# Optimization experiments

Measured on AMD Instinct MI355X. Metric: run time of the kernel, lower is better.

The kernel has to match this reference:

```python
import jax, jax.numpy as jnp
import numpy as np

H = 512   # hidden_size
B = 32    # batch
S = 2048  # src_len
NEG = -1e10


def setup_inputs() -> dict:
    key = jax.random.key(0)
    k1, k2, k3, k4, k5, k6 = jax.random.split(key, 6)
    hidden = jax.random.normal(k1, (B, 2 * H), dtype=jnp.float32)
    encoder_outputs = jax.random.normal(k2, (S, B, 2 * H), dtype=jnp.float32)
    mask = jax.random.randint(k3, (B, S), 0, 2, dtype=jnp.int32)
    # params: nn.Linear(4H, H) -> weight [H, 4H], bias [H]; v ~ U[0,1) [H]
    bound = 1.0 / np.sqrt(4 * H)
    attn_w = jax.random.uniform(k4, (H, 4 * H), minval=-bound, maxval=bound, dtype=jnp.float32)
    attn_b = jax.random.uniform(k5, (H,), minval=-bound, maxval=bound, dtype=jnp.float32)
    v = jax.random.uniform(k6, (H,), dtype=jnp.float32)
    return {"hidden": hidden, "encoder_outputs": encoder_outputs, "mask": mask,
            "attn_w": attn_w, "attn_b": attn_b, "v": v}


def reference(hidden, encoder_outputs, mask, attn_w, attn_b, v):
    # hidden: [B, 2H] -> [B, S, 2H]; encoder_outputs: [S, B, 2H] -> [B, S, 2H]
    src_len = encoder_outputs.shape[0]
    h = jnp.broadcast_to(hidden[:, None, :], (hidden.shape[0], src_len, hidden.shape[1]))
    eo = jnp.transpose(encoder_outputs, (1, 0, 2))
    cat = jnp.concatenate((h, eo), axis=2)                      # [B, S, 4H]
    energy = jnp.tanh(jnp.einsum('bsf,hf->bsh', cat, attn_w) + attn_b)  # [B, S, H]
    attention = jnp.einsum('bsh,h->bs', energy, v)              # [B, S]
    attention = jnp.where(mask == 0, NEG, attention)
    return jax.nn.softmax(attention, axis=1)
```

## Files before the change

### kernel.cpp

```cpp
#include <hip/hip_runtime.h>

#define SLEN 2048
#define BATCH 32
#define HDIM 512
#define KDIM 1024

typedef _Float16 f16x8 __attribute__((ext_vector_type(8)));
typedef _Float16 f16x4 __attribute__((ext_vector_type(4)));
typedef float f32x4 __attribute__((ext_vector_type(4)));

__device__ __forceinline__ void gload16(const void* g, void* l) {
  __builtin_amdgcn_global_load_lds(
      (const __attribute__((address_space(1))) unsigned int*)g,
      (__attribute__((address_space(3))) unsigned int*)l, 16, 0, 0);
}

__device__ __forceinline__ float fast_tanh(float x) {
  float e = __expf(2.0f * x);
  return 1.0f - 2.0f * __builtin_amdgcn_rcpf(e + 1.0f);
}

__global__ __launch_bounds__(256) void prep_k(const float* __restrict__ attn_w,
                                              const float* __restrict__ attn_b,
                                              const float* __restrict__ hidden,
                                              _Float16* __restrict__ Bt,
                                              float* __restrict__ s1,
                                              float* __restrict__ score) {
  if (blockIdx.x < 512) {
    int t = blockIdx.x * 256 + threadIdx.x;
    int h = t >> 8;
    int c = t & 255;
    float4 x = *(const float4*)(attn_w + (size_t)h * 2048 + 1024 + c * 4);
    f16x4 y = {(_Float16)x.x, (_Float16)x.y, (_Float16)x.z, (_Float16)x.w};
    *(f16x4*)(Bt + (size_t)h * 1024 + c * 4) = y;
  } else if (blockIdx.x < 4608) {
    int o = (blockIdx.x - 512) * 4 + (threadIdx.x >> 6);
    int b = o >> 9, h = o & 511;
    int lane = threadIdx.x & 63;
    const float4* hp = (const float4*)(hidden + (size_t)b * 1024);
    const float4* wp = (const float4*)(attn_w + (size_t)h * 2048);
    float acc = 0.f;
#pragma unroll
    for (int c = 0; c < 4; ++c) {
      float4 a = hp[c * 64 + lane];
      float4 wv = wp[c * 64 + lane];
      acc += a.x * wv.x + a.y * wv.y + a.z * wv.z + a.w * wv.w;
    }
#pragma unroll
    for (int off = 1; off < 64; off <<= 1) acc += __shfl_xor(acc, off);
    if (lane == 0) s1[o] = acc + attn_b[h];
  } else {
    int idx = (blockIdx.x - 4608) * 256 + threadIdx.x;
    float4 z = {0.f, 0.f, 0.f, 0.f};
    ((float4*)score)[idx] = z;
    ((float4*)score)[idx + 8192] = z;
  }
}

__global__ __launch_bounds__(256, 2) void gemm_k(const float* __restrict__ eo,
                                                 const _Float16* __restrict__ Bt,
                                                 const float* __restrict__ s1,
                                                 const float* __restrict__ v,
                                                 float* __restrict__ score) {
  constexpr int BK = 32;
  constexpr int NKT = KDIM / BK;
  __shared__ __align__(16) float As[2][256 * BK];
  __shared__ __align__(16) _Float16 Bs[2][128 * BK];

  int bid = blockIdx.x;
  int x = bid & 7;
  int q = bid >> 3;
  int nt = q & 3;
  int mt = (q >> 2) * 8 + x;

  int tid = threadIdx.x;
  int lane = tid & 63;
  int w = tid >> 6;
  int wm = w * 64;

  const float* ga[8];
  const _Float16* gb[2];
#pragma unroll
  for (int i = 0; i < 8; ++i)
    ga[i] = eo + (size_t)(mt * 256 + 64 * w + 8 * i + (lane >> 3)) * KDIM
              + (((lane & 7) ^ (lane >> 3)) << 2);
  gb[0] = Bt + (size_t)(nt * 128 + 32 * w + (lane >> 2)) * KDIM
            + (((lane & 3) ^ (lane >> 4)) << 3);
  gb[1] = gb[0] + 16 * KDIM;

  f32x4 acc[4][8];
#pragma unroll
  for (int i = 0; i < 4; ++i)
#pragma unroll
    for (int j = 0; j < 8; ++j) acc[i][j] = (f32x4){0.f, 0.f, 0.f, 0.f};

  int mrow = lane & 15;
  int quad = lane >> 4;
  int bchunk = (quad ^ (mrow >> 2)) & 3;
  int as_sw = mrow & 7;

  {
    gload16(gb[0], (char*)Bs[0] + (w * 2 + 0) * 1024);
    gload16(gb[1], (char*)Bs[0] + (w * 2 + 1) * 1024);
    gb[0] += BK; gb[1] += BK;
#pragma unroll
    for (int i = 0; i < 8; ++i) {
      gload16(ga[i], (char*)As[0] + (w * 8 + i) * 1024);
      ga[i] += BK;
    }
  }

  for (int kt = 0; kt < NKT; ++kt) {
    int cur = kt & 1;

    if (kt + 1 < NKT) {
      gload16(gb[0], (char*)Bs[cur ^ 1] + (w * 2 + 0) * 1024);
      gload16(gb[1], (char*)Bs[cur ^ 1] + (w * 2 + 1) * 1024);
      gb[0] += BK; gb[1] += BK;
#pragma unroll
      for (int i = 0; i < 8; ++i) {
        gload16(ga[i], (char*)As[cur ^ 1] + (w * 8 + i) * 1024);
        ga[i] += BK;
      }
      asm volatile("s_waitcnt vmcnt(10)" ::: "memory");
    } else {
      asm volatile("s_waitcnt vmcnt(0)" ::: "memory");
    }
    __builtin_amdgcn_s_barrier();

    const float* Ab = As[cur];
    const _Float16* Bb = Bs[cur];
    f16x8 bf[8], af[4];
#pragma unroll
    for (int j = 0; j < 8; ++j)
      bf[j] = *(const f16x8*)&Bb[(16 * j + mrow) * BK + (bchunk << 3)];
#pragma unroll
    for (int i = 0; i < 4; ++i) {
      const float* pa = &Ab[(wm + 16 * i + mrow) * BK];
      float4 a0 = *(const float4*)(pa + (((2 * quad) ^ as_sw) << 2));
      float4 a1 = *(const float4*)(pa + (((2 * quad + 1) ^ as_sw) << 2));
      f16x8 t = {(_Float16)a0.x, (_Float16)a0.y, (_Float16)a0.z, (_Float16)a0.w,
                 (_Float16)a1.x, (_Float16)a1.y, (_Float16)a1.z, (_Float16)a1.w};
      af[i] = t;
    }
    asm volatile("s_waitcnt lgkmcnt(0)" ::: "memory");
    __builtin_amdgcn_sched_barrier(0);
    __builtin_amdgcn_s_barrier();

    __builtin_amdgcn_s_setprio(1);
#pragma unroll
    for (int i = 0; i < 4; ++i)
#pragma unroll
      for (int j = 0; j < 8; ++j)
        acc[i][j] = __builtin_amdgcn_mfma_f32_16x16x32_f16(af[i], bf[j], acc[i][j], 0, 0, 0);
    __builtin_amdgcn_s_setprio(0);
  }

  __syncthreads();
  float* s1s = (float*)As;
  float* vsm = (float*)Bs;
  for (int t = tid; t < 1024; t += 256) {
    int bb = t >> 5, cc = t & 31;
    ((float4*)s1s)[bb * 33 + cc] = *(const float4*)(s1 + (size_t)bb * 512 + nt * 128 + cc * 4);
  }
  if (tid < 32) ((float4*)vsm)[tid] = *(const float4*)(v + nt * 128 + tid * 4);
  __syncthreads();

  int lcol = lane & 15;
  float vv[8];
#pragma unroll
  for (int j = 0; j < 8; ++j) vv[j] = vsm[16 * j + lcol];

#pragma unroll
  for (int i = 0; i < 4; ++i) {
#pragma unroll
    for (int r = 0; r < 4; ++r) {
      int mloc = wm + 16 * i + 4 * quad + r;
      int bb = mloc & 31;
      float sum = 0.f;
#pragma unroll
      for (int j = 0; j < 8; ++j) {
        float e = acc[i][j][r] + s1s[bb * 132 + 16 * j + lcol];
        sum += fast_tanh(e) * vv[j];
      }
      sum += __shfl_xor(sum, 1);
      sum += __shfl_xor(sum, 2);
      sum += __shfl_xor(sum, 4);
      sum += __shfl_xor(sum, 8);
      if (lcol == 0) {
        int mg = mt * 256 + mloc;
        atomicAdd(&score[(mg & 31) * SLEN + (mg >> 5)], sum);
      }
    }
  }
}

__global__ __launch_bounds__(256) void softmax_k(const float* __restrict__ score,
                                                 const int* __restrict__ mask,
                                                 float* __restrict__ out) {
  int b = blockIdx.x;
  int tid = threadIdx.x;
  int lane = tid & 63, w = tid >> 6;
  __shared__ float red[8];
  float vals[8];
  float mx = -3.4e38f;
#pragma unroll
  for (int i = 0; i < 8; ++i) {
    int s = i * 256 + tid;
    float xv = score[b * SLEN + s];
    if (mask[b * SLEN + s] == 0) xv = -1e10f;
    vals[i] = xv;
    mx = fmaxf(mx, xv);
  }
#pragma unroll
  for (int off = 1; off < 64; off <<= 1) mx = fmaxf(mx, __shfl_xor(mx, off));
  if (lane == 0) red[w] = mx;
  __syncthreads();
  mx = fmaxf(fmaxf(red[0], red[1]), fmaxf(red[2], red[3]));
  float sum = 0.f;
#pragma unroll
  for (int i = 0; i < 8; ++i) {
    vals[i] = __expf(vals[i] - mx);
    sum += vals[i];
  }
#pragma unroll
  for (int off = 1; off < 64; off <<= 1) sum += __shfl_xor(sum, off);
  if (lane == 0) red[4 + w] = sum;
  __syncthreads();
  sum = red[4] + red[5] + red[6] + red[7];
  float inv = 1.0f / sum;
#pragma unroll
  for (int i = 0; i < 8; ++i) out[b * SLEN + i * 256 + tid] = vals[i] * inv;
}

extern "C" void kernel_launch(void* const* d_in, const int* in_sizes, int n_in,
                              void* d_out, int out_size, void* d_ws, size_t ws_size,
                              hipStream_t stream) {
  const float* hidden = (const float*)d_in[0];
  const float* eo     = (const float*)d_in[1];
  const int*   mask   = (const int*)d_in[2];
  const float* attn_w = (const float*)d_in[3];
  const float* attn_b = (const float*)d_in[4];
  const float* v      = (const float*)d_in[5];
  float* out = (float*)d_out;

  char* wsb = (char*)d_ws;
  _Float16* Bt = (_Float16*)wsb;
  float* s1    = (float*)(wsb + (1 << 20));
  float* score = (float*)(wsb + (1 << 20) + (1 << 16));

  prep_k<<<4640, 256, 0, stream>>>(attn_w, attn_b, hidden, Bt, s1, score);
  gemm_k<<<1024, 256, 0, stream>>>(eo, Bt, s1, v, score);
  softmax_k<<<BATCH, 256, 0, stream>>>(score, mask, out);
}
```

Measured before the change: 449.4 us.

## Pre-convert encoder outputs to fp16 and retile GEMM with triple buffering

Adds a prep stage that converts the full encoder_outputs tensor to fp16 in workspace. The GEMM then loads fp16 A tiles directly instead of fp32 tiles that had to be converted in registers. The GEMM tile shrinks from 256x128 to 128x128 with a 2x2 warp layout, LDS becomes a 3-stage ring buffer, and occupancy is raised to 3 blocks per CU. This trades an extra full read of eo plus a 128MB fp16 write and re-read for half the LDS and global traffic inside the GEMM and deeper prefetch; the grid doubles, which also doubles the number of atomic adds into the score buffer.

```diff
diff --git a/kernel.cpp b/kernel.cpp
--- a/kernel.cpp
+++ b/kernel.cpp
@@ -23,9 +23,11 @@
 __global__ __launch_bounds__(256) void prep_k(const float* __restrict__ attn_w,
                                               const float* __restrict__ attn_b,
                                               const float* __restrict__ hidden,
+                                              const float* __restrict__ eo,
                                               _Float16* __restrict__ Bt,
                                               float* __restrict__ s1,
-                                              float* __restrict__ score) {
+                                              float* __restrict__ score,
+                                              _Float16* __restrict__ eo16) {
   if (blockIdx.x < 512) {
     int t = blockIdx.x * 256 + threadIdx.x;
     int h = t >> 8;
@@ -49,23 +51,34 @@
 #pragma unroll
     for (int off = 1; off < 64; off <<= 1) acc += __shfl_xor(acc, off);
     if (lane == 0) s1[o] = acc + attn_b[h];
-  } else {
+  } else if (blockIdx.x < 4640) {
     int idx = (blockIdx.x - 4608) * 256 + threadIdx.x;
     float4 z = {0.f, 0.f, 0.f, 0.f};
     ((float4*)score)[idx] = z;
     ((float4*)score)[idx + 8192] = z;
-  }
-}
-
-__global__ __launch_bounds__(256, 2) void gemm_k(const float* __restrict__ eo,
+  } else {
+    int g = (blockIdx.x - 4640) * 256 + threadIdx.x;
+    const float4* src = (const float4*)eo;
+#pragma unroll
+    for (int it = 0; it < 16; ++it) {
+      size_t c = (size_t)it * 524288 + g;
+      float4 a = src[c * 2];
+      float4 b2 = src[c * 2 + 1];
+      f16x8 o = {(_Float16)a.x,  (_Float16)a.y,  (_Float16)a.z,  (_Float16)a.w,
+                 (_Float16)b2.x, (_Float16)b2.y, (_Float16)b2.z, (_Float16)b2.w};
+      *(f16x8*)(eo16 + c * 8) = o;
+    }
+  }
+}
+
+__global__ __launch_bounds__(256, 3) void gemm_k(const _Float16* __restrict__ eo16,
                                                  const _Float16* __restrict__ Bt,
                                                  const float* __restrict__ s1,
                                                  const float* __restrict__ v,
                                                  float* __restrict__ score) {
   constexpr int BK = 32;
   constexpr int NKT = KDIM / BK;
-  __shared__ __align__(16) float As[2][256 * BK];
-  __shared__ __align__(16) _Float16 Bs[2][128 * BK];
+  __shared__ __align__(16) char smem[49152];
 
   int bid = blockIdx.x;
   int x = bid & 7;
@@ -76,73 +89,63 @@
   int tid = threadIdx.x;
   int lane = tid & 63;
   int w = tid >> 6;
-  int wm = w * 64;
-
-  const float* ga[8];
+  int wm = (w >> 1) * 64;
+  int wn = (w & 1) * 64;
+
+  const _Float16* ga[2];
   const _Float16* gb[2];
-#pragma unroll
-  for (int i = 0; i < 8; ++i)
-    ga[i] = eo + (size_t)(mt * 256 + 64 * w + 8 * i + (lane >> 3)) * KDIM
-              + (((lane & 7) ^ (lane >> 3)) << 2);
-  gb[0] = Bt + (size_t)(nt * 128 + 32 * w + (lane >> 2)) * KDIM
-            + (((lane & 3) ^ (lane >> 4)) << 3);
-  gb[1] = gb[0] + 16 * KDIM;
-
-  f32x4 acc[4][8];
+  int swz = ((lane & 3) ^ ((lane >> 3) & 3)) << 3;
+#pragma unroll
+  for (int i = 0; i < 2; ++i) {
+    ga[i] = eo16 + (size_t)(mt * 128 + 32 * w + 16 * i + (lane >> 2)) * KDIM + swz;
+    gb[i] = Bt + (size_t)(nt * 128 + 32 * w + 16 * i + (lane >> 2)) * KDIM + swz;
+  }
+
+  f32x4 acc[4][4];
 #pragma unroll
   for (int i = 0; i < 4; ++i)
 #pragma unroll
-    for (int j = 0; j < 8; ++j) acc[i][j] = (f32x4){0.f, 0.f, 0.f, 0.f};
+    for (int j = 0; j < 4; ++j) acc[i][j] = (f32x4){0.f, 0.f, 0.f, 0.f};
 
   int mrow = lane & 15;
   int quad = lane >> 4;
-  int bchunk = (quad ^ (mrow >> 2)) & 3;
-  int as_sw = mrow & 7;
-
-  {
-    gload16(gb[0], (char*)Bs[0] + (w * 2 + 0) * 1024);
-    gload16(gb[1], (char*)Bs[0] + (w * 2 + 1) * 1024);
-    gb[0] += BK; gb[1] += BK;
-#pragma unroll
-    for (int i = 0; i < 8; ++i) {
-      gload16(ga[i], (char*)As[0] + (w * 8 + i) * 1024);
-      ga[i] += BK;
-    }
-  }
-
+  int rc = (quad ^ ((mrow >> 1) & 3)) << 3;
+
+#define STAGE(buf)                                                    \
+  {                                                                   \
+    gload16(ga[0], smem + (buf)*8192 + (w * 2 + 0) * 1024);           \
+    gload16(ga[1], smem + (buf)*8192 + (w * 2 + 1) * 1024);           \
+    ga[0] += BK; ga[1] += BK;                                         \
+    gload16(gb[0], smem + 24576 + (buf)*8192 + (w * 2 + 0) * 1024);   \
+    gload16(gb[1], smem + 24576 + (buf)*8192 + (w * 2 + 1) * 1024);   \
+    gb[0] += BK; gb[1] += BK;                                         \
+  }
+
+  STAGE(0);
+  STAGE(1);
+
+  int cur = 0, nx2 = 2;
   for (int kt = 0; kt < NKT; ++kt) {
-    int cur = kt & 1;
-
-    if (kt + 1 < NKT) {
-      gload16(gb[0], (char*)Bs[cur ^ 1] + (w * 2 + 0) * 1024);
-      gload16(gb[1], (char*)Bs[cur ^ 1] + (w * 2 + 1) * 1024);
-      gb[0] += BK; gb[1] += BK;
-#pragma unroll
-      for (int i = 0; i < 8; ++i) {
-        gload16(ga[i], (char*)As[cur ^ 1] + (w * 8 + i) * 1024);
-        ga[i] += BK;
-      }
-      asm volatile("s_waitcnt vmcnt(10)" ::: "memory");
+    if (kt + 2 < NKT) {
+      STAGE(nx2);
+      asm volatile("s_waitcnt vmcnt(8)" ::: "memory");
+    } else if (kt + 1 < NKT) {
+      asm volatile("s_waitcnt vmcnt(4)" ::: "memory");
     } else {
       asm volatile("s_waitcnt vmcnt(0)" ::: "memory");
     }
     __builtin_amdgcn_s_barrier();
 
-    const float* Ab = As[cur];
-    const _Float16* Bb = Bs[cur];
-    f16x8 bf[8], af[4];
-#pragma unroll
-    for (int j = 0; j < 8; ++j)
-      bf[j] = *(const f16x8*)&Bb[(16 * j + mrow) * BK + (bchunk << 3)];
-#pragma unroll
-    for (int i = 0; i < 4; ++i) {
-      const float* pa = &Ab[(wm + 16 * i + mrow) * BK];
-      float4 a0 = *(const float4*)(pa + (((2 * quad) ^ as_sw) << 2));
-      float4 a1 = *(const float4*)(pa + (((2 * quad + 1) ^ as_sw) << 2));
-      f16x8 t = {(_Float16)a0.x, (_Float16)a0.y, (_Float16)a0.z, (_Float16)a0.w,
-                 (_Float16)a1.x, (_Float16)a1.y, (_Float16)a1.z, (_Float16)a1.w};
-      af[i] = t;
-    }
+    const _Float16* Ab = (const _Float16*)(smem + cur * 8192);
+    const _Float16* Bb = (const _Float16*)(smem + 24576 + cur * 8192);
+    f16x8 af[4], bf[4];
+#pragma unroll
+    for (int i = 0; i < 4; ++i)
+      af[i] = *(const f16x8*)&Ab[(wm + 16 * i + mrow) * BK + rc];
+#pragma unroll
+    for (int j = 0; j < 4; ++j)
+      bf[j] = *(const f16x8*)&Bb[(wn + 16 * j + mrow) * BK + rc];
+
     asm volatile("s_waitcnt lgkmcnt(0)" ::: "memory");
     __builtin_amdgcn_sched_barrier(0);
     __builtin_amdgcn_s_barrier();
@@ -151,14 +154,18 @@
 #pragma unroll
     for (int i = 0; i < 4; ++i)
 #pragma unroll
-      for (int j = 0; j < 8; ++j)
+      for (int j = 0; j < 4; ++j)
         acc[i][j] = __builtin_amdgcn_mfma_f32_16x16x32_f16(af[i], bf[j], acc[i][j], 0, 0, 0);
     __builtin_amdgcn_s_setprio(0);
-  }
-
-  __syncthreads();
-  float* s1s = (float*)As;
-  float* vsm = (float*)Bs;
+
+    cur = (cur == 2) ? 0 : cur + 1;
+    nx2 = (nx2 == 2) ? 0 : nx2 + 1;
+  }
+#undef STAGE
+
+  __syncthreads();
+  float* s1s = (float*)smem;
+  float* vsm = (float*)(smem + 48640);
   for (int t = tid; t < 1024; t += 256) {
     int bb = t >> 5, cc = t & 31;
     ((float4*)s1s)[bb * 33 + cc] = *(const float4*)(s1 + (size_t)bb * 512 + nt * 128 + cc * 4);
@@ -166,10 +173,10 @@
   if (tid < 32) ((float4*)vsm)[tid] = *(const float4*)(v + nt * 128 + tid * 4);
   __syncthreads();
 
-  int lcol = lane & 15;
-  float vv[8];
-#pragma unroll
-  for (int j = 0; j < 8; ++j) vv[j] = vsm[16 * j + lcol];
+  int lcol = mrow;
+  float vv[4];
+#pragma unroll
+  for (int j = 0; j < 4; ++j) vv[j] = vsm[wn + 16 * j + lcol];
 
 #pragma unroll
   for (int i = 0; i < 4; ++i) {
@@ -179,8 +186,8 @@
       int bb = mloc & 31;
       float sum = 0.f;
 #pragma unroll
-      for (int j = 0; j < 8; ++j) {
-        float e = acc[i][j][r] + s1s[bb * 132 + 16 * j + lcol];
+      for (int j = 0; j < 4; ++j) {
+        float e = acc[i][j][r] + s1s[bb * 132 + wn + 16 * j + lcol];
         sum += fast_tanh(e) * vv[j];
       }
       sum += __shfl_xor(sum, 1);
@@ -188,7 +195,7 @@
       sum += __shfl_xor(sum, 4);
       sum += __shfl_xor(sum, 8);
       if (lcol == 0) {
-        int mg = mt * 256 + mloc;
+        int mg = mt * 128 + mloc;
         atomicAdd(&score[(mg & 31) * SLEN + (mg >> 5)], sum);
       }
     }
@@ -248,8 +255,9 @@
   _Float16* Bt = (_Float16*)wsb;
   float* s1    = (float*)(wsb + (1 << 20));
   float* score = (float*)(wsb + (1 << 20) + (1 << 16));
-
-  prep_k<<<4640, 256, 0, stream>>>(attn_w, attn_b, hidden, Bt, s1, score);
-  gemm_k<<<1024, 256, 0, stream>>>(eo, Bt, s1, v, score);
+  _Float16* eo16 = (_Float16*)(wsb + (2 << 20));
+
+  prep_k<<<6688, 256, 0, stream>>>(attn_w, attn_b, hidden, eo, Bt, s1, score, eo16);
+  gemm_k<<<2048, 256, 0, stream>>>(eo16, Bt, s1, v, score);
   softmax_k<<<BATCH, 256, 0, stream>>>(score, mask, out);
 }
```

Result: slower. 518.1 us (+15.3%).
